# Optimization experiments

Measured on AMD Instinct MI355X. Metric: run time of the kernel, lower is better.

The kernel has to match this reference:

```python
import jax, jax.numpy as jnp
import numpy as np

NUM_SAMPLES = 50      # init kwarg num_samples
EPS = 1e-08           # init kwarg epsilon
PENALTY = 1e-4        # probability penalty weight in forward term
REV_SCALE = 0.1       # reverse-term scaling
CHUNK = 1000          # chunk size for online 1-NN min reduction


def _barycenters(vertices, faces):
    # vertices: [N,3], faces: [F,3] -> [F,3]
    return vertices[faces].mean(axis=1)


def _euclid_dist_matrix(p1, p2):
    # p1: [A,3], p2: [B,3] -> [A,B] Euclidean distances (torch.cdist p=2)
    d2 = (jnp.sum(p1 * p1, axis=-1, keepdims=True)
          - 2.0 * p1 @ p2.T
          + jnp.sum(p2 * p2, axis=-1)[None, :])
    return jnp.sqrt(jnp.maximum(d2, 0.0))


def setup_inputs() -> dict:
    key = jax.random.key(0)
    k0, k1, k2, k3, k4 = jax.random.split(key, 5)
    original_vertices = jax.random.normal(k0, (20000, 3), dtype=jnp.float32)
    original_faces = jax.random.randint(k1, (30000, 3), 0, 20000)
    simplified_vertices = jax.random.normal(k2, (4000, 3), dtype=jnp.float32)
    simplified_faces = jax.random.randint(k3, (5000, 3), 0, 4000)
    face_probabilities = jax.random.uniform(k4, (5000,), dtype=jnp.float32)
    return {
        "original_vertices": original_vertices,
        "original_faces": original_faces,
        "simplified_vertices": simplified_vertices,
        "simplified_faces": simplified_faces,
        "face_probabilities": face_probabilities,
    }


def reference(original_vertices, original_faces, simplified_vertices,
              simplified_faces, face_probabilities):
    n_sf = simplified_faces.shape[0]
    # pad/truncate face_probabilities to number of simplified faces (static shapes)
    fp = jnp.pad(face_probabilities,
                 (0, max(0, n_sf - face_probabilities.shape[0])))[:n_sf]

    # ---- forward term: barycenter cdist + row-min ----
    sb = _barycenters(simplified_vertices, simplified_faces)   # [Fs,3]
    ob = _barycenters(original_vertices, original_faces)       # [Fo,3]
    dist = _euclid_dist_matrix(sb, ob)                         # [Fs,Fo]
    min_d = dist.min(axis=1)                                   # [Fs]
    forward_term = jnp.sum(fp * min_d) + PENALTY * jnp.sum(1.0 - fp)

    # ---- reverse term: barycentric sampling + 1-NN to original vertices ----
    rk1, rk2 = jax.random.split(jax.random.key(42))
    sqrt_r1 = jnp.sqrt(jax.random.uniform(rk1, (n_sf, NUM_SAMPLES, 1)))
    r2 = jax.random.uniform(rk2, (n_sf, NUM_SAMPLES, 1))
    fv = simplified_vertices[simplified_faces]                 # [Fs,3,3]
    a = 1.0 - sqrt_r1
    b = sqrt_r1 * (1.0 - r2)
    c = sqrt_r1 * r2
    samples = (a * fv[:, None, 0] + b * fv[:, None, 1]
               + c * fv[:, None, 2]).reshape(-1, 3)            # [Fs*S,3]

    tv = original_vertices
    tv2 = jnp.sum(tv * tv, axis=-1)                            # [Nov]

    def chunk_min(pts):  # pts: [CHUNK,3] -> [CHUNK] min Euclid distance
        d2 = (jnp.sum(pts * pts, axis=-1, keepdims=True)
              - 2.0 * pts @ tv.T + tv2[None, :])
        return jnp.sqrt(jnp.maximum(d2.min(axis=1), 0.0))

    n_pts = samples.shape[0]
    dists = jax.lax.map(chunk_min,
                        samples.reshape(n_pts // CHUNK, CHUNK, 3)).reshape(-1)
    scaled = dists / (dists.max() + EPS) * REV_SCALE
    reverse_term = jnp.sum(jnp.repeat(fp, NUM_SAMPLES) * scaled)

    return forward_term + reverse_term
```

## Files before the change

kernel.cpp:

```cpp
#include <hip/hip_runtime.h>
#include <stdint.h>
#include <float.h>

#define NUM_SAMPLES 50
#define EPSF 1e-8f
#define PENALTY 1e-4f
#define REV_SCALE 0.1f

#define G1 32
#define G1LO -5.0f
#define G1HI 5.0f
#define NCELL1 (G1*G1*G1)
#define G2 32
#define G2LO -3.5f
#define G2HI 3.5f
#define NCELL2 (G2*G2*G2)

#define NTOTALL (NCELL1 + NCELL2)
#define SCAN_BLOCKS (NTOTALL / 1024)
static_assert(NTOTALL % 1024 == 0, "scan tiling");

#define GS 8
#define QBLOCKS 4096

#define ACC_FLOATS 4096

__device__ __forceinline__ uint32_t rotl32(uint32_t v, int d) {
  return (v << d) | (v >> (32 - d));
}

__device__ __forceinline__ void threefry2x32(uint32_t k0, uint32_t k1,
                                             uint32_t x0, uint32_t x1,
                                             uint32_t& o0, uint32_t& o1) {
  const uint32_t k2 = k0 ^ k1 ^ 0x1BD11BDAu;
  x0 += k0; x1 += k1;
#define TF_ROUND(r) { x0 += x1; x1 = rotl32(x1, (r)); x1 ^= x0; }
  TF_ROUND(13) TF_ROUND(15) TF_ROUND(26) TF_ROUND(6)
  x0 += k1; x1 += k2 + 1u;
  TF_ROUND(17) TF_ROUND(29) TF_ROUND(16) TF_ROUND(24)
  x0 += k2; x1 += k0 + 2u;
  TF_ROUND(13) TF_ROUND(15) TF_ROUND(26) TF_ROUND(6)
  x0 += k0; x1 += k1 + 3u;
  TF_ROUND(17) TF_ROUND(29) TF_ROUND(16) TF_ROUND(24)
  x0 += k1; x1 += k2 + 4u;
  TF_ROUND(13) TF_ROUND(15) TF_ROUND(26) TF_ROUND(6)
  x0 += k2; x1 += k0 + 5u;
#undef TF_ROUND
  o0 = x0; o1 = x1;
}

__device__ __forceinline__ float bits_to_uniform(uint32_t bits) {
  return __uint_as_float((bits >> 9) | 0x3f800000u) - 1.0f;
}

__device__ __forceinline__ float jax_uniform_at(uint32_t k0, uint32_t k1, uint32_t idx) {
  uint32_t o0, o1;
  threefry2x32(k0, k1, 0u, idx, o0, o1);
  return bits_to_uniform(o0 ^ o1);
}

__device__ __forceinline__ int cell_coord(float p, float lo, float invh, int G) {
  int i = (int)floorf((p - lo) * invh);
  return min(max(i, 0), G - 1);
}

__device__ __forceinline__ float4 gen_sample(int id, const float* __restrict__ sv,
                                             const int* __restrict__ sfc,
                                             const float* __restrict__ fp, int NFP) {
  int face = id / NUM_SAMPLES;
  uint32_t a0, a1, b0, b1;
  threefry2x32(0u, 42u, 0u, 0u, a0, a1);
  threefry2x32(0u, 42u, 0u, 1u, b0, b1);
  float r1 = jax_uniform_at(a0, a1, (uint32_t)id);
  float r2 = jax_uniform_at(b0, b1, (uint32_t)id);
  float sr1 = sqrtf(r1);
  float ca = 1.0f - sr1;
  float cb = sr1 * (1.0f - r2);
  float cc = sr1 * r2;
  int va = sfc[3*face], vb = sfc[3*face+1], vc = sfc[3*face+2];
  float px = ca*sv[3*va]   + cb*sv[3*vb]   + cc*sv[3*vc];
  float py = ca*sv[3*va+1] + cb*sv[3*vb+1] + cc*sv[3*vc+1];
  float pz = ca*sv[3*va+2] + cb*sv[3*vb+2] + cc*sv[3*vc+2];
  float w = (face < NFP) ? fp[face] : 0.0f;
  return make_float4(px, py, pz, w);
}

__global__ __launch_bounds__(256) void prep_kernel(
    const float* __restrict__ ov, const int* __restrict__ ofc,
    const float* __restrict__ sv, const int* __restrict__ sfc,
    float4* __restrict__ ob4, float4* __restrict__ sb4, float4* __restrict__ ov4,
    int* __restrict__ cnt, int NOF, int NSF, int NOV) {
  int i = blockIdx.x * blockDim.x + threadIdx.x;
  if (i >= NOF + NSF + NOV) return;
  if (i < NOF) {
    int a = ofc[3*i], b = ofc[3*i+1], c = ofc[3*i+2];
    float x = (ov[3*a]   + ov[3*b]   + ov[3*c])   / 3.0f;
    float y = (ov[3*a+1] + ov[3*b+1] + ov[3*c+1]) / 3.0f;
    float z = (ov[3*a+2] + ov[3*b+2] + ov[3*c+2]) / 3.0f;
    ob4[i] = make_float4(x, y, z, x*x + y*y + z*z);
    const float invh = (float)G2 / (G2HI - G2LO);
    int cx = cell_coord(x, G2LO, invh, G2);
    int cy = cell_coord(y, G2LO, invh, G2);
    int cz = cell_coord(z, G2LO, invh, G2);
    atomicAdd(&cnt[NCELL1 + (cz*G2 + cy)*G2 + cx], 1);
  } else if (i < NOF + NSF) {
    int j = i - NOF;
    int a = sfc[3*j], b = sfc[3*j+1], c = sfc[3*j+2];
    float x = (sv[3*a]   + sv[3*b]   + sv[3*c])   / 3.0f;
    float y = (sv[3*a+1] + sv[3*b+1] + sv[3*c+1]) / 3.0f;
    float z = (sv[3*a+2] + sv[3*b+2] + sv[3*c+2]) / 3.0f;
    sb4[j] = make_float4(x, y, z, x*x + y*y + z*z);
  } else {
    int j = i - NOF - NSF;
    float x = ov[3*j], y = ov[3*j+1], z = ov[3*j+2];
    ov4[j] = make_float4(x, y, z, x*x + y*y + z*z);
    const float invh = (float)G1 / (G1HI - G1LO);
    int cx = cell_coord(x, G1LO, invh, G1);
    int cy = cell_coord(y, G1LO, invh, G1);
    int cz = cell_coord(z, G1LO, invh, G1);
    atomicAdd(&cnt[(cz*G1 + cy)*G1 + cx], 1);
  }
}

__global__ __launch_bounds__(256) void scan_kernel(
    const int4* __restrict__ cnt4, unsigned long long* __restrict__ gsum,
    int* __restrict__ cs, int* __restrict__ cur) {
  __shared__ int lds[256];
  __shared__ int wsum[4];
  __shared__ int boffS;
  int t = threadIdx.x;
  int gid = blockIdx.x * 256 + t;
  int4 c = cnt4[gid];
  int s01 = c.x + c.y;
  int tsum = s01 + c.z + c.w;
  lds[t] = tsum;
  __syncthreads();
  for (int d = 1; d < 256; d <<= 1) {
    int u = (t >= d) ? lds[t - d] : 0;
    __syncthreads();
    lds[t] += u;
    __syncthreads();
  }
  int incl = lds[t];
  int agg  = lds[255];
  if (t == 0)
    atomicExch(&gsum[blockIdx.x], (1ULL << 63) | (unsigned long long)(unsigned)agg);
  int pre = 0;
  if (t < (int)blockIdx.x) {
    unsigned long long v;
    while (!((v = __hip_atomic_load(&gsum[t], __ATOMIC_RELAXED,
                                    __HIP_MEMORY_SCOPE_AGENT)) >> 63)) { }
    pre = (int)(v & 0xFFFFFFFFULL);
  }
  for (int o = 32; o > 0; o >>= 1) pre += __shfl_down(pre, o);
  if ((t & 63) == 0) wsum[t >> 6] = pre;
  __syncthreads();
  if (t == 0) boffS = wsum[0] + wsum[1] + wsum[2] + wsum[3];
  __syncthreads();
  int base = boffS + incl - tsum;
  int4 o4;
  o4.x = base;
  o4.y = base + c.x;
  o4.z = base + s01;
  o4.w = base + s01 + c.z;
  ((int4*)cs)[gid] = o4;
  ((int4*)cur)[gid] = o4;
  if (blockIdx.x == gridDim.x - 1 && t == 255) cs[NTOTALL] = boffS + incl;
}

__global__ __launch_bounds__(256) void scatter_kernel(
    const float4* __restrict__ ov4, const float4* __restrict__ ob4,
    int* __restrict__ cur, float4* __restrict__ sorted, int NOV, int NOF) {
  int i = blockIdx.x * blockDim.x + threadIdx.x;
  if (i >= NOV + NOF) return;
  float4 p; int c;
  if (i < NOV) {
    p = ov4[i];
    const float invh = (float)G1 / (G1HI - G1LO);
    int cx = cell_coord(p.x, G1LO, invh, G1);
    int cy = cell_coord(p.y, G1LO, invh, G1);
    int cz = cell_coord(p.z, G1LO, invh, G1);
    c = (cz*G1 + cy)*G1 + cx;
  } else {
    p = ob4[i - NOV];
    const float invh = (float)G2 / (G2HI - G2LO);
    int cx = cell_coord(p.x, G2LO, invh, G2);
    int cy = cell_coord(p.y, G2LO, invh, G2);
    int cz = cell_coord(p.z, G2LO, invh, G2);
    c = NCELL1 + (cz*G2 + cy)*G2 + cx;
  }
  int idx = atomicAdd(&cur[c], 1);
  sorted[idx] = p;
}

__device__ __forceinline__ float group_min(float v) {
  for (int o = GS / 2; o > 0; o >>= 1) v = fminf(v, __shfl_xor(v, o, GS));
  return v;
}

__device__ float nn_group(float px, float py, float pz, float q2,
                          const int* __restrict__ cs, const float4* __restrict__ pts,
                          int G, float lo, float h, int cellofs, int lane) {
  const float invh = 1.0f / h;
  int ix = cell_coord(px, lo, invh, G);
  int iy = cell_coord(py, lo, invh, G);
  int iz = cell_coord(pz, lo, invh, G);
  float wxm = fmaxf(px - (lo + (float)ix * h), 0.0f);
  float wxp = fmaxf((lo + (float)(ix + 1) * h) - px, 0.0f);
  float wym = fmaxf(py - (lo + (float)iy * h), 0.0f);
  float wyp = fmaxf((lo + (float)(iy + 1) * h) - py, 0.0f);
  float wzm = fmaxf(pz - (lo + (float)iz * h), 0.0f);
  float wzp = fmaxf((lo + (float)(iz + 1) * h) - pz, 0.0f);
  float wmin = fminf(fminf(fminf(wxm, wxp), fminf(wym, wyp)), fminf(wzm, wzp));

  float m2x = -2.0f*px, m2y = -2.0f*py, m2z = -2.0f*pz;
  float best = FLT_MAX;

  int x0 = max(ix - 1, 0), x1 = min(ix + 1, G - 1);

  int   sA[9], eA[9];
  float rb2[9];
  {
    const float dzo0 = wzm, dzo2 = wzp;
    const float dyo0 = wym, dyo2 = wyp;
#pragma unroll
    for (int k = 0; k < 9; ++k) {
      const int dzi = k / 3, dyi = k % 3;
      int zz = min(max(iz + dzi - 1, 0), G - 1);
      int yy = min(max(iy + dyi - 1, 0), G - 1);
      int rowbase = cellofs + (zz * G + yy) * G;
      sA[k] = cs[rowbase + x0];
      eA[k] = cs[rowbase + x1 + 1];
      float dz = (dzi == 0) ? dzo0 : (dzi == 2) ? dzo2 : 0.0f;
      float dy = (dyi == 0) ? dyo0 : (dyi == 2) ? dyo2 : 0.0f;
      rb2[k] = dz * dz + dy * dy;
    }
  }
  for (int i = sA[4] + lane; i < eA[4]; i += GS) {
    float4 v = pts[i];
    best = fminf(best, fmaf(v.z, m2z, fmaf(v.y, m2y, fmaf(v.x, m2x, v.w))));
  }
  float bmind2 = group_min(best) + q2;
#pragma unroll
  for (int k = 0; k < 9; ++k) {
    if (k == 4) continue;
    if (rb2[k] < bmind2) {
      for (int i = sA[k] + lane; i < eA[k]; i += GS) {
        float4 v = pts[i];
        best = fminf(best, fmaf(v.z, m2z, fmaf(v.y, m2y, fmaf(v.x, m2x, v.w))));
      }
    }
  }
  float bmin = group_min(best);
  {
    float bd = h + wmin;
    if (bmin + q2 <= bd * bd) return bmin;
  }

  best = bmin;
  for (int r = 2; r < G; ++r) {
    float bestd2 = group_min(best) + q2;
    float bd = (float)(r - 1) * h + wmin;
    if (bestd2 <= bd * bd) break;
    int z0 = max(iz - r, 0), z1 = min(iz + r, G - 1);
    int y0 = max(iy - r, 0), y1 = min(iy + r, G - 1);
    int rx0 = max(ix - r, 0), rx1 = min(ix + r, G - 1);
    float dxm = (float)(r - 1) * h + wxm;
    float dxp = (float)(r - 1) * h + wxp;
    for (int zz = z0; zz <= z1; ++zz) {
      int oz = zz - iz;
      int adz = abs(oz);
      float dz = (oz > 0) ? (float)(oz - 1) * h + wzp
               : (oz < 0) ? (float)(-oz - 1) * h + wzm : 0.0f;
      float dz2 = dz * dz;
      if (dz2 >= bestd2) continue;
      for (int yy = y0; yy <= y1; ++yy) {
        int oy = yy - iy;
        int ady = abs(oy);
        float dy = (oy > 0) ? (float)(oy - 1) * h + wyp
                 : (oy < 0) ? (float)(-oy - 1) * h + wym : 0.0f;
        float rowd2 = dz2 + dy * dy;
        if (rowd2 >= bestd2) continue;
        int rowbase = cellofs + (zz*G + yy)*G;
        if (adz == r || ady == r) {
          int s = cs[rowbase + rx0];
          int e = cs[rowbase + rx1 + 1];
          for (int i = s + lane; i < e; i += GS) {
            float4 v = pts[i];
            best = fminf(best, fmaf(v.z, m2z, fmaf(v.y, m2y, fmaf(v.x, m2x, v.w))));
          }
        } else {
          if (ix - r >= 0 && rowd2 + dxm * dxm < bestd2) {
            int cc = rowbase + ix - r;
            int s = cs[cc], e = cs[cc + 1];
            for (int i = s + lane; i < e; i += GS) {
              float4 v = pts[i];
              best = fminf(best, fmaf(v.z, m2z, fmaf(v.y, m2y, fmaf(v.x, m2x, v.w))));
            }
          }
          if (ix + r <= G - 1 && rowd2 + dxp * dxp < bestd2) {
            int cc = rowbase + ix + r;
            int s = cs[cc], e = cs[cc + 1];
            for (int i = s + lane; i < e; i += GS) {
              float4 v = pts[i];
              best = fminf(best, fmaf(v.z, m2z, fmaf(v.y, m2y, fmaf(v.x, m2x, v.w))));
            }
          }
        }
      }
    }
  }
  return group_min(best);
}

__global__ __launch_bounds__(256) void query_kernel(
    const float* __restrict__ fp, const float4* __restrict__ sb4,
    const float* __restrict__ sv, const int* __restrict__ sfc,
    const int* __restrict__ cs, const float4* __restrict__ sorted,
    float* __restrict__ acc, float* __restrict__ out,
    int NSF, int NFP, int nsamp) {
  const float h1 = (G1HI - G1LO) / (float)G1;
  const float h2 = (G2HI - G2LO) / (float)G2;
  int lane = threadIdx.x & (GS - 1);
  int grpInBlk = threadIdx.x / GS;
  const int grpsPerBlk = 256 / GS;
  int totalGroups = NSF + nsamp;
  float facc = 0.0f, racc = 0.0f, rmaxv = 0.0f;
  for (int g = blockIdx.x * grpsPerBlk + grpInBlk; g < totalGroups;
       g += gridDim.x * grpsPerBlk) {
    if (g < NSF) {
      float4 s = sb4[g];
      float best = nn_group(s.x, s.y, s.z, s.w, cs, sorted, G2, G2LO, h2, NCELL1, lane);
      if (lane == 0) {
        float mind = sqrtf(fmaxf(best + s.w, 0.0f));
        float p = (g < NFP) ? fp[g] : 0.0f;
        facc += p * mind;
      }
    } else {
      int sid = g - NSF;
      float4 s = gen_sample(sid, sv, sfc, fp, NFP);
      float q2 = s.x*s.x + s.y*s.y + s.z*s.z;
      float best = nn_group(s.x, s.y, s.z, q2, cs, sorted, G1, G1LO, h1, 0, lane);
      if (lane == 0) {
        float d = sqrtf(fmaxf(best + q2, 0.0f));
        racc += s.w * d;
        rmaxv = fmaxf(rmaxv, d);
      }
    }
  }
  __shared__ float sF[4], sR[4], sM[4];
  __shared__ int isLast;
  __shared__ float stash[4];
  for (int o = 32; o > 0; o >>= 1) {
    facc += __shfl_down(facc, o);
    racc += __shfl_down(racc, o);
    rmaxv = fmaxf(rmaxv, __shfl_down(rmaxv, o));
  }
  int wid = threadIdx.x >> 6;
  if ((threadIdx.x & 63) == 0) { sF[wid] = facc; sR[wid] = racc; sM[wid] = rmaxv; }
  __syncthreads();
  if (threadIdx.x == 0) {
    float tf = sF[0] + sF[1] + sF[2] + sF[3];
    float tr = sR[0] + sR[1] + sR[2] + sR[3];
    float tm = fmaxf(fmaxf(sM[0], sM[1]), fmaxf(sM[2], sM[3]));
    int slot = (blockIdx.x & 63) * 16;
    atomicAdd(&acc[slot], tf);
    atomicAdd(&acc[1024 + slot], tr);
    atomicMax((int*)acc + 2048 + slot, __float_as_int(tm));
    __threadfence();
    int old = atomicAdd((int*)acc + 3072, 1);
    isLast = (old == (int)gridDim.x - 1) ? 1 : 0;
  }
  __syncthreads();
  if (!isLast) return;

  __shared__ float red[256];
  int t = threadIdx.x;
  float fsum = 0.0f, rsum = 0.0f, rmx = 0.0f;
  if (t < 64)        fsum = atomicAdd(&acc[t * 16], 0.0f);
  else if (t < 128)  rsum = atomicAdd(&acc[1024 + (t - 64) * 16], 0.0f);
  else if (t < 192)  rmx  = __int_as_float(atomicMax((int*)acc + 2048 + (t - 128) * 16, 0));
  float sfp = 0.0f;
  for (int i = t; i < NSF; i += 256) sfp += (i < NFP) ? fp[i] : 0.0f;

  red[t] = fsum; __syncthreads();
  for (int o = 128; o > 0; o >>= 1) { if (t < o) red[t] += red[t + o]; __syncthreads(); }
  if (t == 0) stash[0] = red[0];
  __syncthreads();
  red[t] = rsum; __syncthreads();
  for (int o = 128; o > 0; o >>= 1) { if (t < o) red[t] += red[t + o]; __syncthreads(); }
  if (t == 0) stash[1] = red[0];
  __syncthreads();
  red[t] = rmx; __syncthreads();
  for (int o = 128; o > 0; o >>= 1) { if (t < o) red[t] = fmaxf(red[t], red[t + o]); __syncthreads(); }
  if (t == 0) stash[2] = red[0];
  __syncthreads();
  red[t] = sfp; __syncthreads();
  for (int o = 128; o > 0; o >>= 1) { if (t < o) red[t] += red[t + o]; __syncthreads(); }
  if (t == 0) {
    float fwd = stash[0] + PENALTY * ((float)NSF - red[0]);
    float rev = stash[1] * (REV_SCALE / (stash[2] + EPSF));
    out[0] = fwd + rev;
  }
}

extern "C" void kernel_launch(void* const* d_in, const int* in_sizes, int n_in,
                              void* d_out, int out_size, void* d_ws, size_t ws_size,
                              hipStream_t stream) {
  const float* ov  = (const float*)d_in[0];
  const int*   ofc = (const int*)  d_in[1];
  const float* sv  = (const float*)d_in[2];
  const int*   sfc = (const int*)  d_in[3];
  const float* fp  = (const float*)d_in[4];
  float* out = (float*)d_out;

  int NOV = in_sizes[0] / 3;
  int NOF = in_sizes[1] / 3;
  int NSF = in_sizes[3] / 3;
  int NFP = in_sizes[4];
  int nsamp = NSF * NUM_SAMPLES;

  char* w = (char*)d_ws;
  float* acc = (float*)w;                       w += ACC_FLOATS * 4;
  unsigned long long* gsum = (unsigned long long*)w; w += 2048;
  int*   cnt = (int*)w;                         w += (size_t)NTOTALL * 4;
  size_t zeroBytes = (size_t)(w - (char*)d_ws);
  int*   cs  = (int*)w;                         w += (size_t)(NTOTALL + 16) * 4;
  int*   cur = (int*)w;                         w += (size_t)NTOTALL * 4;
  float4* ob4    = (float4*)w;  w += (size_t)NOF * 16;
  float4* sb4    = (float4*)w;  w += (size_t)NSF * 16;
  float4* ov4    = (float4*)w;  w += (size_t)NOV * 16;
  float4* sorted = (float4*)w;  w += (size_t)(NOV + NOF) * 16;

  hipMemsetAsync(d_ws, 0, zeroBytes, stream);

  int total = NOF + NSF + NOV;
  hipLaunchKernelGGL(prep_kernel, dim3((total + 255) / 256), dim3(256), 0, stream,
                     ov, ofc, sv, sfc, ob4, sb4, ov4, cnt, NOF, NSF, NOV);

  hipLaunchKernelGGL(scan_kernel, dim3(SCAN_BLOCKS), dim3(256), 0, stream,
                     (const int4*)cnt, gsum, cs, cur);

  hipLaunchKernelGGL(scatter_kernel, dim3((NOV + NOF + 255) / 256), dim3(256), 0, stream,
                     ov4, ob4, cur, sorted, NOV, NOF);

  hipLaunchKernelGGL(query_kernel, dim3(QBLOCKS), dim3(256), 0, stream,
                     fp, sb4, sv, sfc, cs, sorted, acc, out, NSF, NFP, nsamp);
}
```

Measured before the change: 210.7 us.

## Fuse prep, scan and scatter into one persistent kernel with grid barriers

```diff
diff --git a/kernel.cpp b/kernel.cpp
--- a/kernel.cpp
+++ b/kernel.cpp
@@ -17,8 +17,9 @@
 #define NCELL2 (G2*G2*G2)
 
 #define NTOTALL (NCELL1 + NCELL2)
-#define SCAN_BLOCKS (NTOTALL / 1024)
-static_assert(NTOTALL % 1024 == 0, "scan tiling");
+#define SCAN_BLOCKS 64
+static_assert(NTOTALL == SCAN_BLOCKS * 1024, "scan tiling");
+#define BGRID 256
 
 #define GS 8
 #define QBLOCKS 4096
@@ -85,112 +86,135 @@
   return make_float4(px, py, pz, w);
 }
 
-__global__ __launch_bounds__(256) void prep_kernel(
+__device__ __forceinline__ void abarrier(int* ctr, int target) {
+  __syncthreads();
+  if (threadIdx.x == 0) {
+    __hip_atomic_fetch_add(ctr, 1, __ATOMIC_RELEASE, __HIP_MEMORY_SCOPE_AGENT);
+    while (__hip_atomic_load(ctr, __ATOMIC_ACQUIRE, __HIP_MEMORY_SCOPE_AGENT) < target) {}
+  }
+  __syncthreads();
+}
+
+__global__ __launch_bounds__(256) void build_kernel(
     const float* __restrict__ ov, const int* __restrict__ ofc,
     const float* __restrict__ sv, const int* __restrict__ sfc,
-    float4* __restrict__ ob4, float4* __restrict__ sb4, float4* __restrict__ ov4,
-    int* __restrict__ cnt, int NOF, int NSF, int NOV) {
-  int i = blockIdx.x * blockDim.x + threadIdx.x;
-  if (i >= NOF + NSF + NOV) return;
-  if (i < NOF) {
-    int a = ofc[3*i], b = ofc[3*i+1], c = ofc[3*i+2];
-    float x = (ov[3*a]   + ov[3*b]   + ov[3*c])   / 3.0f;
-    float y = (ov[3*a+1] + ov[3*b+1] + ov[3*c+1]) / 3.0f;
-    float z = (ov[3*a+2] + ov[3*b+2] + ov[3*c+2]) / 3.0f;
-    ob4[i] = make_float4(x, y, z, x*x + y*y + z*z);
-    const float invh = (float)G2 / (G2HI - G2LO);
-    int cx = cell_coord(x, G2LO, invh, G2);
-    int cy = cell_coord(y, G2LO, invh, G2);
-    int cz = cell_coord(z, G2LO, invh, G2);
-    atomicAdd(&cnt[NCELL1 + (cz*G2 + cy)*G2 + cx], 1);
-  } else if (i < NOF + NSF) {
-    int j = i - NOF;
-    int a = sfc[3*j], b = sfc[3*j+1], c = sfc[3*j+2];
-    float x = (sv[3*a]   + sv[3*b]   + sv[3*c])   / 3.0f;
-    float y = (sv[3*a+1] + sv[3*b+1] + sv[3*c+1]) / 3.0f;
-    float z = (sv[3*a+2] + sv[3*b+2] + sv[3*c+2]) / 3.0f;
-    sb4[j] = make_float4(x, y, z, x*x + y*y + z*z);
-  } else {
-    int j = i - NOF - NSF;
-    float x = ov[3*j], y = ov[3*j+1], z = ov[3*j+2];
-    ov4[j] = make_float4(x, y, z, x*x + y*y + z*z);
-    const float invh = (float)G1 / (G1HI - G1LO);
-    int cx = cell_coord(x, G1LO, invh, G1);
-    int cy = cell_coord(y, G1LO, invh, G1);
-    int cz = cell_coord(z, G1LO, invh, G1);
-    atomicAdd(&cnt[(cz*G1 + cy)*G1 + cx], 1);
-  }
-}
-
-__global__ __launch_bounds__(256) void scan_kernel(
-    const int4* __restrict__ cnt4, unsigned long long* __restrict__ gsum,
-    int* __restrict__ cs, int* __restrict__ cur) {
+    int* __restrict__ cnt, unsigned long long* __restrict__ gsum,
+    int* __restrict__ bar, int* __restrict__ cs, int* __restrict__ cur,
+    float4* __restrict__ sb4, float4* __restrict__ sorted,
+    int NOF, int NSF, int NOV) {
+  const int t = threadIdx.x;
+  const int bid = (int)blockIdx.x;
+  const int gtid = bid * 256 + t;
+  const int nth = BGRID * 256;
+
   __shared__ int lds[256];
   __shared__ int wsum[4];
   __shared__ int boffS;
-  int t = threadIdx.x;
-  int gid = blockIdx.x * 256 + t;
-  int4 c = cnt4[gid];
-  int s01 = c.x + c.y;
-  int tsum = s01 + c.z + c.w;
-  lds[t] = tsum;
-  __syncthreads();
-  for (int d = 1; d < 256; d <<= 1) {
-    int u = (t >= d) ? lds[t - d] : 0;
+
+  for (int i = gtid; i < NOF + NSF + NOV; i += nth) {
+    if (i < NOF) {
+      int a = ofc[3*i], b = ofc[3*i+1], c = ofc[3*i+2];
+      float x = (ov[3*a]   + ov[3*b]   + ov[3*c])   / 3.0f;
+      float y = (ov[3*a+1] + ov[3*b+1] + ov[3*c+1]) / 3.0f;
+      float z = (ov[3*a+2] + ov[3*b+2] + ov[3*c+2]) / 3.0f;
+      const float invh = (float)G2 / (G2HI - G2LO);
+      int cx = cell_coord(x, G2LO, invh, G2);
+      int cy = cell_coord(y, G2LO, invh, G2);
+      int cz = cell_coord(z, G2LO, invh, G2);
+      atomicAdd(&cnt[NCELL1 + (cz*G2 + cy)*G2 + cx], 1);
+    } else if (i < NOF + NSF) {
+      int j = i - NOF;
+      int a = sfc[3*j], b = sfc[3*j+1], c = sfc[3*j+2];
+      float x = (sv[3*a]   + sv[3*b]   + sv[3*c])   / 3.0f;
+      float y = (sv[3*a+1] + sv[3*b+1] + sv[3*c+1]) / 3.0f;
+      float z = (sv[3*a+2] + sv[3*b+2] + sv[3*c+2]) / 3.0f;
+      sb4[j] = make_float4(x, y, z, x*x + y*y + z*z);
+    } else {
+      int j = i - NOF - NSF;
+      float x = ov[3*j], y = ov[3*j+1], z = ov[3*j+2];
+      const float invh = (float)G1 / (G1HI - G1LO);
+      int cx = cell_coord(x, G1LO, invh, G1);
+      int cy = cell_coord(y, G1LO, invh, G1);
+      int cz = cell_coord(z, G1LO, invh, G1);
+      atomicAdd(&cnt[(cz*G1 + cy)*G1 + cx], 1);
+    }
+  }
+  abarrier(&bar[0], BGRID);
+
+  if (bid < SCAN_BLOCKS) {
+    int gid = bid * 256 + t;
+    int4 c;
+    c.x = __hip_atomic_load(&cnt[4*gid+0], __ATOMIC_RELAXED, __HIP_MEMORY_SCOPE_AGENT);
+    c.y = __hip_atomic_load(&cnt[4*gid+1], __ATOMIC_RELAXED, __HIP_MEMORY_SCOPE_AGENT);
+    c.z = __hip_atomic_load(&cnt[4*gid+2], __ATOMIC_RELAXED, __HIP_MEMORY_SCOPE_AGENT);
+    c.w = __hip_atomic_load(&cnt[4*gid+3], __ATOMIC_RELAXED, __HIP_MEMORY_SCOPE_AGENT);
+    int s01 = c.x + c.y;
+    int tsum = s01 + c.z + c.w;
+    lds[t] = tsum;
     __syncthreads();
-    lds[t] += u;
+    for (int d = 1; d < 256; d <<= 1) {
+      int u = (t >= d) ? lds[t - d] : 0;
+      __syncthreads();
+      lds[t] += u;
+      __syncthreads();
+    }
+    int incl = lds[t];
+    int agg  = lds[255];
+    if (t == 0)
+      atomicExch(&gsum[bid], (1ULL << 63) | (unsigned long long)(unsigned)agg);
+    int pre = 0;
+    if (t < bid) {
+      unsigned long long v;
+      while (!((v = __hip_atomic_load(&gsum[t], __ATOMIC_RELAXED,
+                                      __HIP_MEMORY_SCOPE_AGENT)) >> 63)) { }
+      pre = (int)(v & 0xFFFFFFFFULL);
+    }
+    for (int o = 32; o > 0; o >>= 1) pre += __shfl_down(pre, o);
+    if ((t & 63) == 0) wsum[t >> 6] = pre;
     __syncthreads();
-  }
-  int incl = lds[t];
-  int agg  = lds[255];
-  if (t == 0)
-    atomicExch(&gsum[blockIdx.x], (1ULL << 63) | (unsigned long long)(unsigned)agg);
-  int pre = 0;
-  if (t < (int)blockIdx.x) {
-    unsigned long long v;
-    while (!((v = __hip_atomic_load(&gsum[t], __ATOMIC_RELAXED,
-                                    __HIP_MEMORY_SCOPE_AGENT)) >> 63)) { }
-    pre = (int)(v & 0xFFFFFFFFULL);
-  }
-  for (int o = 32; o > 0; o >>= 1) pre += __shfl_down(pre, o);
-  if ((t & 63) == 0) wsum[t >> 6] = pre;
-  __syncthreads();
-  if (t == 0) boffS = wsum[0] + wsum[1] + wsum[2] + wsum[3];
-  __syncthreads();
-  int base = boffS + incl - tsum;
-  int4 o4;
-  o4.x = base;
-  o4.y = base + c.x;
-  o4.z = base + s01;
-  o4.w = base + s01 + c.z;
-  ((int4*)cs)[gid] = o4;
-  ((int4*)cur)[gid] = o4;
-  if (blockIdx.x == gridDim.x - 1 && t == 255) cs[NTOTALL] = boffS + incl;
-}
-
-__global__ __launch_bounds__(256) void scatter_kernel(
-    const float4* __restrict__ ov4, const float4* __restrict__ ob4,
-    int* __restrict__ cur, float4* __restrict__ sorted, int NOV, int NOF) {
-  int i = blockIdx.x * blockDim.x + threadIdx.x;
-  if (i >= NOV + NOF) return;
-  float4 p; int c;
-  if (i < NOV) {
-    p = ov4[i];
-    const float invh = (float)G1 / (G1HI - G1LO);
-    int cx = cell_coord(p.x, G1LO, invh, G1);
-    int cy = cell_coord(p.y, G1LO, invh, G1);
-    int cz = cell_coord(p.z, G1LO, invh, G1);
-    c = (cz*G1 + cy)*G1 + cx;
-  } else {
-    p = ob4[i - NOV];
-    const float invh = (float)G2 / (G2HI - G2LO);
-    int cx = cell_coord(p.x, G2LO, invh, G2);
-    int cy = cell_coord(p.y, G2LO, invh, G2);
-    int cz = cell_coord(p.z, G2LO, invh, G2);
-    c = NCELL1 + (cz*G2 + cy)*G2 + cx;
-  }
-  int idx = atomicAdd(&cur[c], 1);
-  sorted[idx] = p;
+    if (t == 0) boffS = wsum[0] + wsum[1] + wsum[2] + wsum[3];
+    __syncthreads();
+    int base = boffS + incl - tsum;
+    int4 o4;
+    o4.x = base;
+    o4.y = base + c.x;
+    o4.z = base + s01;
+    o4.w = base + s01 + c.z;
+    ((int4*)cs)[gid] = o4;
+    __hip_atomic_store(&cur[4*gid+0], o4.x, __ATOMIC_RELAXED, __HIP_MEMORY_SCOPE_AGENT);
+    __hip_atomic_store(&cur[4*gid+1], o4.y, __ATOMIC_RELAXED, __HIP_MEMORY_SCOPE_AGENT);
+    __hip_atomic_store(&cur[4*gid+2], o4.z, __ATOMIC_RELAXED, __HIP_MEMORY_SCOPE_AGENT);
+    __hip_atomic_store(&cur[4*gid+3], o4.w, __ATOMIC_RELAXED, __HIP_MEMORY_SCOPE_AGENT);
+    if (bid == SCAN_BLOCKS - 1 && t == 255) cs[NTOTALL] = boffS + incl;
+  }
+  abarrier(&bar[1], BGRID);
+
+  for (int i = gtid; i < NOV + NOF; i += nth) {
+    float4 p; int c;
+    if (i < NOV) {
+      float x = ov[3*i], y = ov[3*i+1], z = ov[3*i+2];
+      p = make_float4(x, y, z, x*x + y*y + z*z);
+      const float invh = (float)G1 / (G1HI - G1LO);
+      int cx = cell_coord(x, G1LO, invh, G1);
+      int cy = cell_coord(y, G1LO, invh, G1);
+      int cz = cell_coord(z, G1LO, invh, G1);
+      c = (cz*G1 + cy)*G1 + cx;
+    } else {
+      int j = i - NOV;
+      int a = ofc[3*j], b = ofc[3*j+1], cc2 = ofc[3*j+2];
+      float x = (ov[3*a]   + ov[3*b]   + ov[3*cc2])   / 3.0f;
+      float y = (ov[3*a+1] + ov[3*b+1] + ov[3*cc2+1]) / 3.0f;
+      float z = (ov[3*a+2] + ov[3*b+2] + ov[3*cc2+2]) / 3.0f;
+      p = make_float4(x, y, z, x*x + y*y + z*z);
+      const float invh = (float)G2 / (G2HI - G2LO);
+      int cx = cell_coord(x, G2LO, invh, G2);
+      int cy = cell_coord(y, G2LO, invh, G2);
+      int cz = cell_coord(z, G2LO, invh, G2);
+      c = NCELL1 + (cz*G2 + cy)*G2 + cx;
+    }
+    int idx = atomicAdd(&cur[c], 1);
+    sorted[idx] = p;
+  }
 }
 
 __device__ __forceinline__ float group_min(float v) {
@@ -423,26 +447,19 @@
   char* w = (char*)d_ws;
   float* acc = (float*)w;                       w += ACC_FLOATS * 4;
   unsigned long long* gsum = (unsigned long long*)w; w += 2048;
+  int*   bar = (int*)w;                         w += 64;
   int*   cnt = (int*)w;                         w += (size_t)NTOTALL * 4;
   size_t zeroBytes = (size_t)(w - (char*)d_ws);
   int*   cs  = (int*)w;                         w += (size_t)(NTOTALL + 16) * 4;
   int*   cur = (int*)w;                         w += (size_t)NTOTALL * 4;
-  float4* ob4    = (float4*)w;  w += (size_t)NOF * 16;
   float4* sb4    = (float4*)w;  w += (size_t)NSF * 16;
-  float4* ov4    = (float4*)w;  w += (size_t)NOV * 16;
   float4* sorted = (float4*)w;  w += (size_t)(NOV + NOF) * 16;
 
   hipMemsetAsync(d_ws, 0, zeroBytes, stream);
 
-  int total = NOF + NSF + NOV;
-  hipLaunchKernelGGL(prep_kernel, dim3((total + 255) / 256), dim3(256), 0, stream,
-                     ov, ofc, sv, sfc, ob4, sb4, ov4, cnt, NOF, NSF, NOV);
-
-  hipLaunchKernelGGL(scan_kernel, dim3(SCAN_BLOCKS), dim3(256), 0, stream,
-                     (const int4*)cnt, gsum, cs, cur);
-
-  hipLaunchKernelGGL(scatter_kernel, dim3((NOV + NOF + 255) / 256), dim3(256), 0, stream,
-                     ov4, ob4, cur, sorted, NOV, NOF);
+  hipLaunchKernelGGL(build_kernel, dim3(BGRID), dim3(256), 0, stream,
+                     ov, ofc, sv, sfc, cnt, gsum, bar, cs, cur, sb4, sorted,
+                     NOF, NSF, NOV);
 
   hipLaunchKernelGGL(query_kernel, dim3(QBLOCKS), dim3(256), 0, stream,
                      fp, sb4, sv, sfc, cs, sorted, acc, out, NSF, NFP, nsamp);
```

Result: slower. 245.2 us (+16.4%).
